# Performance work log

Measured on AMD Instinct MI355X. Metric: run time of the kernel, lower is better.

Reference implementation:

```python
import jax, jax.numpy as jnp
import numpy as np

D_MODEL, D_FF, N_EXPERTS, TOP_K = 1024, 4096, 8, 2

def setup_inputs() -> dict:
    key = jax.random.key(0)
    k0, k1, k2, k3 = jax.random.split(key, 4)
    x = jax.random.normal(k0, (2, 2048, D_MODEL), dtype=jnp.float32)
    Wg = jax.random.normal(k1, (D_MODEL, N_EXPERTS), dtype=jnp.float32) * 0.02
    W1 = jax.random.normal(k2, (N_EXPERTS, D_MODEL, D_FF), dtype=jnp.float32) * 0.02
    b1 = jnp.zeros((N_EXPERTS, D_FF), dtype=jnp.float32)
    W2 = jax.random.normal(k3, (N_EXPERTS, D_FF, D_MODEL), dtype=jnp.float32) * 0.02
    b2 = jnp.zeros((N_EXPERTS, D_MODEL), dtype=jnp.float32)
    return {"x": x, "Wg": Wg, "W1": W1, "b1": b1, "W2": W2, "b2": b2}

def reference(x, Wg, W1, b1, W2, b2):
    B = x.shape[:-1]
    xs = x.reshape(-1, x.shape[-1])                 # [T, D]
    T = xs.shape[0]
    gate_logits = xs @ Wg                           # [T, E]
    weights, sel = jax.lax.top_k(gate_logits, TOP_K)  # [T, k]
    # softmax over the top-k logits, computed in fp32 then cast back (matches F.softmax(dtype=float).type_as)
    weights = jax.nn.softmax(weights.astype(jnp.float32), axis=1).astype(x.dtype)
    # dense all-experts MLP: [E, T, D_FF] -> [E, T, D]
    h = jax.nn.relu(jnp.einsum('td,edf->etf', xs, W1) + b1[:, None, :])
    out_e = jnp.einsum('etf,efd->etd', h, W2) + b2[:, None, :]
    # gather each token's top-k expert outputs and combine with routing weights
    tok = jnp.arange(T)
    picked = out_e[sel, tok[:, None]]               # [T, k, D]
    out = jnp.einsum('tk,tkd->td', weights, picked) # [T, D]
    return out.reshape(*B, x.shape[-1])
```

## Files before the change

### kernel.cpp

```cpp
#include <hip/hip_runtime.h>
#include <cstdint>
#include <cstddef>

#define T_TOKENS 4096
#define DM 1024
#define DF 4096
#define NE 8
#define TOPK 2
#define BK 32
#define MAX_MT 72
#define MSLOTS 8192

typedef short short8 __attribute__((ext_vector_type(8)));
typedef float f32x4 __attribute__((ext_vector_type(4)));

__device__ __forceinline__ unsigned short f2h_bits(float f) {
  _Float16 h = (_Float16)f;
  union { _Float16 h; unsigned short u; } v; v.h = h; return v.u;
}

typedef __attribute__((address_space(3))) void lds_void_t;
typedef __attribute__((address_space(1))) void gvoid_t;
__device__ __forceinline__ void gl_lds16(const void* g, void* l) {
  __builtin_amdgcn_global_load_lds((gvoid_t*)g, (lds_void_t*)l, 16, 0, 0);
}

__global__ void gate_kernel(const float* __restrict__ x, const float* __restrict__ Wg,
                            int* __restrict__ sel, float* __restrict__ wts,
                            int* __restrict__ counts, unsigned short* __restrict__ Xh) {
  int wave = threadIdx.x >> 6, lane = threadIdx.x & 63;
  int t = blockIdx.x * 4 + wave;
  const float* xr = x + (size_t)t * DM;
  unsigned short* xh = Xh + (size_t)t * DM;
  float acc[NE];
#pragma unroll
  for (int e = 0; e < NE; e++) acc[e] = 0.f;
#pragma unroll
  for (int j = 0; j < 4; j++) {
    int d4 = (lane + 64 * j) * 4;
    float4 v = *(const float4*)(xr + d4);
    ushort4 o;
    o.x = f2h_bits(v.x); o.y = f2h_bits(v.y); o.z = f2h_bits(v.z); o.w = f2h_bits(v.w);
    *(ushort4*)(xh + d4) = o;
    const float* wr = Wg + (size_t)d4 * NE;
#pragma unroll
    for (int e = 0; e < NE; e++) acc[e] += v.x * wr[e];
#pragma unroll
    for (int e = 0; e < NE; e++) acc[e] += v.y * wr[NE + e];
#pragma unroll
    for (int e = 0; e < NE; e++) acc[e] += v.z * wr[2 * NE + e];
#pragma unroll
    for (int e = 0; e < NE; e++) acc[e] += v.w * wr[3 * NE + e];
  }
#pragma unroll
  for (int e = 0; e < NE; e++) {
    float v = acc[e];
#pragma unroll
    for (int off = 32; off > 0; off >>= 1) v += __shfl_down(v, off, 64);
    acc[e] = v;
  }
  if (lane == 0) {
    int b0 = 0;
#pragma unroll
    for (int e = 1; e < NE; e++) if (acc[e] > acc[b0]) b0 = e;
    int b1 = (b0 == 0) ? 1 : 0;
#pragma unroll
    for (int e = 0; e < NE; e++) if (e != b0 && acc[e] > acc[b1]) b1 = e;
    float p = expf(acc[b1] - acc[b0]);
    float w0 = 1.f / (1.f + p);
    sel[t * 2] = b0; sel[t * 2 + 1] = b1;
    wts[t * 2] = w0; wts[t * 2 + 1] = p * w0;
    atomicAdd(&counts[b0], 1);
    atomicAdd(&counts[b1], 1);
  }
}

__global__ void scan_kernel(const int* __restrict__ counts, int* __restrict__ offsets,
                            int* __restrict__ tile_off, int* __restrict__ cursors) {
  if (threadIdx.x == 0) {
    int o = 0, to = 0;
    offsets[0] = 0; tile_off[0] = 0;
    for (int e = 0; e < NE; e++) {
      cursors[e] = o;
      o += counts[e];
      to += (counts[e] + 127) >> 7;
      offsets[e + 1] = o;
      tile_off[e + 1] = to;
    }
  }
}

__global__ void scatter_kernel(const int* __restrict__ sel, const float* __restrict__ wts,
                               int* __restrict__ cursors, int* __restrict__ rows,
                               float* __restrict__ rw, int* __restrict__ inv) {
  int t = blockIdx.x * 256 + threadIdx.x;
  if (t >= T_TOKENS) return;
#pragma unroll
  for (int k = 0; k < TOPK; k++) {
    int e = sel[t * 2 + k];
    int slot = atomicAdd(&cursors[e], 1);
    rows[slot] = t;
    rw[slot] = wts[t * 2 + k];
    inv[t * 2 + k] = slot;
  }
}

__global__ void transpose_convert(const float* __restrict__ W1, unsigned short* __restrict__ W1t,
                                  const float* __restrict__ W2, unsigned short* __restrict__ W2t) {
  __shared__ float tile[64 * 65];
  int z = blockIdx.y;
  int R, C;
  const float* inE;
  unsigned short* outE;
  int tidx = blockIdx.x;
  int bx, by;
  if (z < 8) {
    R = DM; C = DF;
    inE = W1 + (size_t)z * DM * DF;
    outE = W1t + (size_t)z * DM * DF;
    bx = tidx % (DF / 64); by = tidx / (DF / 64);
  } else {
    R = DF; C = DM;
    inE = W2 + (size_t)(z - 8) * DM * DF;
    outE = W2t + (size_t)(z - 8) * DM * DF;
    bx = tidx % (DM / 64); by = tidx / (DM / 64);
  }
  int c0 = bx * 64, r0 = by * 64;
  int tid = threadIdx.x;
  int rr = tid >> 4, c4 = (tid & 15) * 4;
#pragma unroll
  for (int it = 0; it < 4; it++) {
    int r = rr + 16 * it;
    float4 v = *(const float4*)(inE + (size_t)(r0 + r) * C + c0 + c4);
    tile[r * 65 + c4 + 0] = v.x;
    tile[r * 65 + c4 + 1] = v.y;
    tile[r * 65 + c4 + 2] = v.z;
    tile[r * 65 + c4 + 3] = v.w;
  }
  __syncthreads();
#pragma unroll
  for (int it = 0; it < 2; it++) {
    int idx = tid + 256 * it;
    int c = idx >> 3, r8 = (idx & 7) * 8;
    short8 val;
#pragma unroll
    for (int j = 0; j < 8; j++) val[j] = (short)f2h_bits(tile[(r8 + j) * 65 + c]);
    *(short8*)(outE + (size_t)(c0 + c) * R + r0 + r8) = val;
  }
}

template <int K, int N, int NT, bool INDIR, bool SECOND>
__global__ __launch_bounds__(256, 4) void moe_gemm(
    const unsigned short* __restrict__ Aall, const unsigned short* __restrict__ Ball,
    unsigned short* __restrict__ Hout, float* __restrict__ Sout,
    const float* __restrict__ bias, const int* __restrict__ counts,
    const int* __restrict__ offsets, const int* __restrict__ tile_off,
    const int* __restrict__ rows, const float* __restrict__ rw) {
  __shared__ __align__(16) unsigned short lds[8704];
  unsigned short* ldsA = lds;
  unsigned short* ldsB = lds + 4096;

  int id = blockIdx.x;
  int nt = id % NT;
  int bx = id / NT;
  int e = 0;
#pragma unroll 1
  while (e < NE && bx >= tile_off[e + 1]) e++;
  if (e >= NE) return;
  int lt = bx - tile_off[e];
  int cnt = counts[e];
  int m0 = lt * 128;
  int rowbase = offsets[e];
  int n0 = nt * 128;

  const unsigned short* Be = Ball + ((size_t)e * N + n0) * K;

  int tid = threadIdx.x;
  int lane = tid & 63, wave = tid >> 6;
  int wm = wave & 1, wn = wave >> 1;

  int rA0 = tid >> 2, rA1 = (256 + tid) >> 2, seg = tid & 3;
  int mA0 = m0 + rA0; if (mA0 >= cnt) mA0 = cnt - 1;
  int mA1 = m0 + rA1; if (mA1 >= cnt) mA1 = cnt - 1;
  size_t ia0 = INDIR ? (size_t)rows[rowbase + mA0] : (size_t)(rowbase + mA0);
  size_t ia1 = INDIR ? (size_t)rows[rowbase + mA1] : (size_t)(rowbase + mA1);
  const unsigned short* srcA0 = Aall + ia0 * K + seg * 8;
  const unsigned short* srcA1 = Aall + ia1 * K + seg * 8;
  const unsigned short* srcB0 = Be + (size_t)rA0 * K + seg * 8;
  const unsigned short* srcB1 = Be + (size_t)rA1 * K + seg * 8;
  unsigned short* dA0 = ldsA + (size_t)tid * 8;
  unsigned short* dA1 = ldsA + (size_t)(256 + tid) * 8;
  unsigned short* dB0 = ldsB + (size_t)tid * 8;
  unsigned short* dB1 = ldsB + (size_t)(256 + tid) * 8;

  f32x4 acc[4][4] = {};

  for (int kk = 0; kk < K; kk += BK) {
    gl_lds16(srcA0 + kk, dA0);
    gl_lds16(srcA1 + kk, dA1);
    gl_lds16(srcB0 + kk, dB0);
    gl_lds16(srcB1 + kk, dB1);
    __syncthreads();

    short8 af[4], bfr[4];
#pragma unroll
    for (int t4 = 0; t4 < 4; t4++) {
      af[t4]  = *(const short8*)(ldsA + (wm * 64 + t4 * 16 + (lane & 15)) * BK + (lane >> 4) * 8);
      bfr[t4] = *(const short8*)(ldsB + (wn * 64 + t4 * 16 + (lane & 15)) * BK + (lane >> 4) * 8);
    }
#pragma unroll
    for (int tm = 0; tm < 4; tm++)
#pragma unroll
      for (int tn = 0; tn < 4; tn++)
        acc[tm][tn] = __builtin_amdgcn_mfma_f32_16x16x32_f16(af[tm], bfr[tn], acc[tm][tn], 0, 0, 0);
    __syncthreads();
  }

  int quad = lane >> 4, c16 = lane & 15;
  if constexpr (!SECOND) {
#pragma unroll 1
    for (int half = 0; half < 2; half++) {
      __syncthreads();
      if (wm == half) {
#pragma unroll
        for (int tm = 0; tm < 4; tm++) {
#pragma unroll
          for (int tn = 0; tn < 4; tn++) {
            int colL = wn * 64 + tn * 16 + c16;
            float b = bias[e * N + n0 + colL];
#pragma unroll
            for (int r = 0; r < 4; r++) {
              int rl = tm * 16 + quad * 4 + r;
              float v = fmaxf(acc[tm][tn][r] + b, 0.f);
              lds[rl * 136 + colL] = f2h_bits(v);
            }
          }
        }
      }
      __syncthreads();
#pragma unroll
      for (int i = 0; i < 4; i++) {
        int idx = tid + 256 * i;
        int row = idx >> 4, c8 = (idx & 15) * 8;
        int grow = m0 + half * 64 + row;
        if (grow < cnt) {
          short8 val = *(const short8*)(lds + row * 136 + c8);
          *(short8*)(Hout + (size_t)(rowbase + grow) * N + n0 + c8) = val;
        }
      }
    }
  } else {
#pragma unroll
    for (int tm = 0; tm < 4; tm++) {
#pragma unroll
      for (int tn = 0; tn < 4; tn++) {
        int gcol = n0 + wn * 64 + tn * 16 + c16;
        float b = bias[e * N + gcol];
#pragma unroll
        for (int r = 0; r < 4; r++) {
          int rl = wm * 64 + tm * 16 + quad * 4 + r;
          if (m0 + rl < cnt) {
            int slot = rowbase + m0 + rl;
            Sout[(size_t)slot * N + gcol] = (acc[tm][tn][r] + b) * rw[slot];
          }
        }
      }
    }
  }
}

__global__ void combine_kernel(const float* __restrict__ S, const int* __restrict__ inv,
                               float* __restrict__ out) {
  int wave = threadIdx.x >> 6, lane = threadIdx.x & 63;
  int t = blockIdx.x * 4 + wave;
  int s0 = inv[t * 2], s1 = inv[t * 2 + 1];
  const float4* a = (const float4*)(S + (size_t)s0 * DM);
  const float4* b = (const float4*)(S + (size_t)s1 * DM);
  float4* o = (float4*)(out + (size_t)t * DM);
#pragma unroll
  for (int j = 0; j < 4; j++) {
    float4 va = a[lane + 64 * j], vb = b[lane + 64 * j];
    float4 vo; vo.x = va.x + vb.x; vo.y = va.y + vb.y; vo.z = va.z + vb.z; vo.w = va.w + vb.w;
    o[lane + 64 * j] = vo;
  }
}

extern "C" void kernel_launch(void* const* d_in, const int* in_sizes, int n_in,
                              void* d_out, int out_size, void* d_ws, size_t ws_size,
                              hipStream_t stream) {
  const float* x  = (const float*)d_in[0];
  const float* Wg = (const float*)d_in[1];
  const float* W1 = (const float*)d_in[2];
  const float* b1 = (const float*)d_in[3];
  const float* W2 = (const float*)d_in[4];
  const float* b2 = (const float*)d_in[5];
  float* out = (float*)d_out;

  char* ws = (char*)d_ws;
  int*   counts   = (int*)(ws + 0);
  int*   cursors  = (int*)(ws + 64);
  int*   offsets  = (int*)(ws + 128);
  int*   tile_off = (int*)(ws + 192);
  int*   sel      = (int*)(ws + 256);
  float* wts      = (float*)(ws + 33024);
  int*   rows     = (int*)(ws + 65792);
  float* rw       = (float*)(ws + 98560);
  int*   inv      = (int*)(ws + 131328);
  unsigned short* Xh  = (unsigned short*)(ws + 164096);
  unsigned short* H   = (unsigned short*)(ws + 8552704);
  unsigned short* W1t = (unsigned short*)(ws + 75661568);
  float*          S   = (float*)(ws + 75661568);
  unsigned short* W2t = (unsigned short*)(ws + 142770432);

  hipMemsetAsync(ws, 0, 128, stream);

  gate_kernel<<<T_TOKENS / 4, 256, 0, stream>>>(x, Wg, sel, wts, counts, Xh);
  scan_kernel<<<1, 64, 0, stream>>>(counts, offsets, tile_off, cursors);
  scatter_kernel<<<T_TOKENS / 256, 256, 0, stream>>>(sel, wts, cursors, rows, rw, inv);
  transpose_convert<<<dim3(1024, 16), 256, 0, stream>>>(W1, W1t, W2, W2t);

  moe_gemm<DM, DF, 32, true, false><<<MAX_MT * 32, 256, 0, stream>>>(
      Xh, W1t, H, nullptr, b1, counts, offsets, tile_off, rows, rw);
  moe_gemm<DF, DM, 8, false, true><<<MAX_MT * 8, 256, 0, stream>>>(
      H, W2t, nullptr, S, b2, counts, offsets, tile_off, rows, rw);

  combine_kernel<<<T_TOKENS / 4, 256, 0, stream>>>(S, inv, out);
}
```

Before: 685.6 us.

## Double-buffer LDS tiles, swizzle LDS layout, and split-K the second expert GEMM

```diff
diff --git a/kernel.cpp b/kernel.cpp
--- a/kernel.cpp
+++ b/kernel.cpp
@@ -149,20 +149,20 @@
   }
 }
 
-template <int K, int N, int NT, bool INDIR, bool SECOND>
+template <int K, int N, int NT, int NSPLIT, bool INDIR, bool SECOND>
 __global__ __launch_bounds__(256, 4) void moe_gemm(
     const unsigned short* __restrict__ Aall, const unsigned short* __restrict__ Ball,
     unsigned short* __restrict__ Hout, float* __restrict__ Sout,
     const float* __restrict__ bias, const int* __restrict__ counts,
     const int* __restrict__ offsets, const int* __restrict__ tile_off,
     const int* __restrict__ rows, const float* __restrict__ rw) {
-  __shared__ __align__(16) unsigned short lds[8704];
-  unsigned short* ldsA = lds;
-  unsigned short* ldsB = lds + 4096;
+  __shared__ __align__(16) unsigned short lds[16384];
 
   int id = blockIdx.x;
   int nt = id % NT;
-  int bx = id / NT;
+  int rest = id / NT;
+  int ks = rest % NSPLIT;
+  int bx = rest / NSPLIT;
   int e = 0;
 #pragma unroll 1
   while (e < NE && bx >= tile_off[e + 1]) e++;
@@ -173,50 +173,73 @@
   int rowbase = offsets[e];
   int n0 = nt * 128;
 
-  const unsigned short* Be = Ball + ((size_t)e * N + n0) * K;
+  const int KS = K / NSPLIT;
+  const int kbeg = ks * KS;
+
+  const unsigned short* Be = Ball + ((size_t)e * N + n0) * K + kbeg;
 
   int tid = threadIdx.x;
   int lane = tid & 63, wave = tid >> 6;
   int wm = wave & 1, wn = wave >> 1;
 
-  int rA0 = tid >> 2, rA1 = (256 + tid) >> 2, seg = tid & 3;
+  int rA0 = tid >> 2, rA1 = (256 + tid) >> 2;
+  int segl = (tid & 3) ^ ((rA0 >> 1) & 3);
   int mA0 = m0 + rA0; if (mA0 >= cnt) mA0 = cnt - 1;
   int mA1 = m0 + rA1; if (mA1 >= cnt) mA1 = cnt - 1;
   size_t ia0 = INDIR ? (size_t)rows[rowbase + mA0] : (size_t)(rowbase + mA0);
   size_t ia1 = INDIR ? (size_t)rows[rowbase + mA1] : (size_t)(rowbase + mA1);
-  const unsigned short* srcA0 = Aall + ia0 * K + seg * 8;
-  const unsigned short* srcA1 = Aall + ia1 * K + seg * 8;
-  const unsigned short* srcB0 = Be + (size_t)rA0 * K + seg * 8;
-  const unsigned short* srcB1 = Be + (size_t)rA1 * K + seg * 8;
-  unsigned short* dA0 = ldsA + (size_t)tid * 8;
-  unsigned short* dA1 = ldsA + (size_t)(256 + tid) * 8;
-  unsigned short* dB0 = ldsB + (size_t)tid * 8;
-  unsigned short* dB1 = ldsB + (size_t)(256 + tid) * 8;
+  const unsigned short* srcA0 = Aall + ia0 * K + kbeg + segl * 8;
+  const unsigned short* srcA1 = Aall + ia1 * K + kbeg + segl * 8;
+  const unsigned short* srcB0 = Be + (size_t)rA0 * K + segl * 8;
+  const unsigned short* srcB1 = Be + (size_t)rA1 * K + segl * 8;
+
+  int quad = lane >> 4, c15 = lane & 15;
+  int sp = ((quad ^ ((c15 >> 1) & 3))) * 8;
+  int aoff[4], boff[4];
+#pragma unroll
+  for (int t4 = 0; t4 < 4; t4++) {
+    aoff[t4] = (wm * 64 + t4 * 16 + c15) * BK + sp;
+    boff[t4] = (wn * 64 + t4 * 16 + c15) * BK + sp;
+  }
 
   f32x4 acc[4][4] = {};
 
-  for (int kk = 0; kk < K; kk += BK) {
-    gl_lds16(srcA0 + kk, dA0);
-    gl_lds16(srcA1 + kk, dA1);
-    gl_lds16(srcB0 + kk, dB0);
-    gl_lds16(srcB1 + kk, dB1);
-    __syncthreads();
-
+  auto stage = [&](int buf, int kk) {
+    unsigned short* base = lds + (buf << 13);
+    gl_lds16(srcA0 + kk, base + (size_t)tid * 8);
+    gl_lds16(srcA1 + kk, base + (size_t)(256 + tid) * 8);
+    gl_lds16(srcB0 + kk, base + 4096 + (size_t)tid * 8);
+    gl_lds16(srcB1 + kk, base + 4096 + (size_t)(256 + tid) * 8);
+  };
+  auto compute = [&](int buf) {
+    const unsigned short* bA = lds + (buf << 13);
+    const unsigned short* bB = bA + 4096;
     short8 af[4], bfr[4];
 #pragma unroll
     for (int t4 = 0; t4 < 4; t4++) {
-      af[t4]  = *(const short8*)(ldsA + (wm * 64 + t4 * 16 + (lane & 15)) * BK + (lane >> 4) * 8);
-      bfr[t4] = *(const short8*)(ldsB + (wn * 64 + t4 * 16 + (lane & 15)) * BK + (lane >> 4) * 8);
+      af[t4]  = *(const short8*)(bA + aoff[t4]);
+      bfr[t4] = *(const short8*)(bB + boff[t4]);
     }
 #pragma unroll
     for (int tm = 0; tm < 4; tm++)
 #pragma unroll
       for (int tn = 0; tn < 4; tn++)
         acc[tm][tn] = __builtin_amdgcn_mfma_f32_16x16x32_f16(af[tm], bfr[tn], acc[tm][tn], 0, 0, 0);
+  };
+
+  stage(0, 0);
+  __syncthreads();
+  const int NK = KS / BK;
+#pragma unroll 1
+  for (int it = 0; it < NK; it += 2) {
+    if (it + 1 < NK) stage(1, (it + 1) * BK);
+    compute(0);
     __syncthreads();
-  }
-
-  int quad = lane >> 4, c16 = lane & 15;
+    if (it + 2 < NK) stage(0, (it + 2) * BK);
+    compute(1);
+    __syncthreads();
+  }
+
   if constexpr (!SECOND) {
 #pragma unroll 1
     for (int half = 0; half < 2; half++) {
@@ -226,7 +249,7 @@
         for (int tm = 0; tm < 4; tm++) {
 #pragma unroll
           for (int tn = 0; tn < 4; tn++) {
-            int colL = wn * 64 + tn * 16 + c16;
+            int colL = wn * 64 + tn * 16 + c15;
             float b = bias[e * N + n0 + colL];
 #pragma unroll
             for (int r = 0; r < 4; r++) {
@@ -250,18 +273,19 @@
       }
     }
   } else {
+    float* So = Sout + (size_t)ks * ((size_t)MSLOTS * N);
 #pragma unroll
     for (int tm = 0; tm < 4; tm++) {
 #pragma unroll
       for (int tn = 0; tn < 4; tn++) {
-        int gcol = n0 + wn * 64 + tn * 16 + c16;
-        float b = bias[e * N + gcol];
+        int gcol = n0 + wn * 64 + tn * 16 + c15;
+        float b = (ks == 0) ? bias[e * N + gcol] : 0.f;
 #pragma unroll
         for (int r = 0; r < 4; r++) {
           int rl = wm * 64 + tm * 16 + quad * 4 + r;
           if (m0 + rl < cnt) {
             int slot = rowbase + m0 + rl;
-            Sout[(size_t)slot * N + gcol] = (acc[tm][tn][r] + b) * rw[slot];
+            So[(size_t)slot * N + gcol] = (acc[tm][tn][r] + b) * rw[slot];
           }
         }
       }
@@ -274,14 +298,22 @@
   int wave = threadIdx.x >> 6, lane = threadIdx.x & 63;
   int t = blockIdx.x * 4 + wave;
   int s0 = inv[t * 2], s1 = inv[t * 2 + 1];
-  const float4* a = (const float4*)(S + (size_t)s0 * DM);
-  const float4* b = (const float4*)(S + (size_t)s1 * DM);
+  const size_t HALF4 = (size_t)MSLOTS * DM / 4;
+  const float4* a0 = (const float4*)S + (size_t)s0 * (DM / 4);
+  const float4* a1 = a0 + HALF4;
+  const float4* b0 = (const float4*)S + (size_t)s1 * (DM / 4);
+  const float4* b1 = b0 + HALF4;
   float4* o = (float4*)(out + (size_t)t * DM);
 #pragma unroll
   for (int j = 0; j < 4; j++) {
-    float4 va = a[lane + 64 * j], vb = b[lane + 64 * j];
-    float4 vo; vo.x = va.x + vb.x; vo.y = va.y + vb.y; vo.z = va.z + vb.z; vo.w = va.w + vb.w;
-    o[lane + 64 * j] = vo;
+    int i = lane + 64 * j;
+    float4 va = a0[i], vb = a1[i], vc = b0[i], vd = b1[i];
+    float4 vo;
+    vo.x = (va.x + vb.x) + (vc.x + vd.x);
+    vo.y = (va.y + vb.y) + (vc.y + vd.y);
+    vo.z = (va.z + vb.z) + (vc.z + vd.z);
+    vo.w = (va.w + vb.w) + (vc.w + vd.w);
+    o[i] = vo;
   }
 }
 
@@ -319,9 +351,9 @@
   scatter_kernel<<<T_TOKENS / 256, 256, 0, stream>>>(sel, wts, cursors, rows, rw, inv);
   transpose_convert<<<dim3(1024, 16), 256, 0, stream>>>(W1, W1t, W2, W2t);
 
-  moe_gemm<DM, DF, 32, true, false><<<MAX_MT * 32, 256, 0, stream>>>(
+  moe_gemm<DM, DF, 32, 1, true, false><<<MAX_MT * 32, 256, 0, stream>>>(
       Xh, W1t, H, nullptr, b1, counts, offsets, tile_off, rows, rw);
-  moe_gemm<DF, DM, 8, false, true><<<MAX_MT * 8, 256, 0, stream>>>(
+  moe_gemm<DF, DM, 8, 2, false, true><<<MAX_MT * 8 * 2, 256, 0, stream>>>(
       H, W2t, nullptr, S, b2, counts, offsets, tile_off, rows, rw);
 
   combine_kernel<<<T_TOKENS / 4, 256, 0, stream>>>(S, inv, out);
```

Result: no change. 687.5 us (+0.3%).
